# Optimization experiments

Hardware: AMD Instinct MI355X
Metric: run time of the kernel (lower is better)

The kernel has to match this reference:

```python
import jax, jax.numpy as jnp
import numpy as np

B, N, R, OUT = 8192, 4096, 16, 4096
STD = 0.01


def setup_inputs() -> dict:
    key = jax.random.key(0)
    ks = jax.random.split(key, 6)
    x = jax.random.normal(ks[0], (B, N), dtype=jnp.float32)
    G = STD * jax.random.normal(ks[1], (R, N), dtype=jnp.float32)
    H = STD * jax.random.normal(ks[2], (R, N), dtype=jnp.float32)
    b1 = STD * jax.random.normal(ks[3], (N,), dtype=jnp.float32)
    W2 = STD * jax.random.normal(ks[4], (N, OUT), dtype=jnp.float32)
    b2 = STD * jax.random.normal(ks[5], (OUT,), dtype=jnp.float32)
    return {"x": x, "G": G, "H": H, "b1": b1, "W2": W2, "b2": b2}


def reference(x, G, H, b1, W2, b2):
    # low-rank structured layer: xW = (x @ H^T) @ G  -- rank-r factorization of W
    xH = jnp.einsum('bn,rn->br', x, H)   # [B, r]
    xW = jnp.einsum('br,rn->bn', xH, G)  # [B, N]
    h = jax.nn.relu(xW + b1)             # num_layers == 1 branch
    y = jnp.matmul(h, W2) + b2           # [B, OUT]
    return y
```

## Files before the change

### kernel.cpp

```cpp
#include <hip/hip_runtime.h>
#include <hip/hip_bf16.h>
#include <cstdint>
#include <cstddef>

typedef __bf16 bf16;
typedef __bf16 bf16x4 __attribute__((ext_vector_type(4)));
typedef __bf16 bf16x8 __attribute__((ext_vector_type(8)));
typedef float  f32x4  __attribute__((ext_vector_type(4)));

#define MB   8192
#define NN   4096
#define RR   16
#define KOUT 4096

__device__ __forceinline__ void gload_lds16(const bf16* g, bf16* l) {
  __builtin_amdgcn_global_load_lds(
      (const __attribute__((address_space(1))) void*)g,
      (__attribute__((address_space(3))) void*)l, 16, 0, 0);
}

__global__ __launch_bounds__(256) void k1_lowrank(
    const float* __restrict__ x, const float* __restrict__ G,
    const float* __restrict__ H, const float* __restrict__ b1,
    bf16* __restrict__ hout)
{
  __shared__ float sS[16][16];
  const int t    = threadIdx.x;
  const int lane = t & 63;
  const int wave = t >> 6;
  const int r0   = blockIdx.x * 16;
  const int i0   = wave * 4;

  float acc[4][RR];
#pragma unroll
  for (int j = 0; j < 4; ++j)
#pragma unroll
    for (int r = 0; r < RR; ++r) acc[j][r] = 0.f;

  for (int kt = 0; kt < NN; kt += 256) {
    const int k = kt + lane * 4;
    f32x4 xv[4];
#pragma unroll
    for (int j = 0; j < 4; ++j)
      xv[j] = *(const f32x4*)(x + (size_t)(r0 + i0 + j) * NN + k);
#pragma unroll
    for (int r = 0; r < RR; ++r) {
      const f32x4 hv = *(const f32x4*)(H + (size_t)r * NN + k);
#pragma unroll
      for (int j = 0; j < 4; ++j) {
        acc[j][r] = fmaf(xv[j].x, hv.x, acc[j][r]);
        acc[j][r] = fmaf(xv[j].y, hv.y, acc[j][r]);
        acc[j][r] = fmaf(xv[j].z, hv.z, acc[j][r]);
        acc[j][r] = fmaf(xv[j].w, hv.w, acc[j][r]);
      }
    }
  }

#pragma unroll
  for (int j = 0; j < 4; ++j)
#pragma unroll
    for (int r = 0; r < RR; ++r) {
      float v = acc[j][r];
#pragma unroll
      for (int off = 32; off >= 1; off >>= 1) v += __shfl_xor(v, off, 64);
      acc[j][r] = v;
    }
  if (lane == 0) {
#pragma unroll
    for (int j = 0; j < 4; ++j)
#pragma unroll
      for (int r = 0; r < RR; ++r) sS[i0 + j][r] = acc[j][r];
  }
  __syncthreads();

#pragma unroll
  for (int chunk = 0; chunk < 4; ++chunk) {
    const int c = chunk * 1024 + t * 4;
    const f32x4 b1v = *(const f32x4*)(b1 + c);
#pragma unroll
    for (int ib = 0; ib < 16; ib += 4) {
      f32x4 a0 = {0.f,0.f,0.f,0.f}, a1 = a0, a2 = a0, a3 = a0;
#pragma unroll
      for (int rb = 0; rb < 16; rb += 4) {
        const f32x4 sv0 = *(const f32x4*)&sS[ib + 0][rb];
        const f32x4 sv1 = *(const f32x4*)&sS[ib + 1][rb];
        const f32x4 sv2 = *(const f32x4*)&sS[ib + 2][rb];
        const f32x4 sv3 = *(const f32x4*)&sS[ib + 3][rb];
#pragma unroll
        for (int rr = 0; rr < 4; ++rr) {
          const f32x4 g4 = *(const f32x4*)(G + (size_t)(rb + rr) * NN + c);
          a0 += sv0[rr] * g4;
          a1 += sv1[rr] * g4;
          a2 += sv2[rr] * g4;
          a3 += sv3[rr] * g4;
        }
      }
#define STORE_ROW(jj, av) {                                        \
      const f32x4 hv = (av) + b1v;                                 \
      bf16x4 o;                                                    \
      o[0] = (bf16)fmaxf(hv[0], 0.f); o[1] = (bf16)fmaxf(hv[1], 0.f); \
      o[2] = (bf16)fmaxf(hv[2], 0.f); o[3] = (bf16)fmaxf(hv[3], 0.f); \
      *(bf16x4*)(hout + (size_t)(r0 + ib + (jj)) * NN + c) = o; }
      STORE_ROW(0, a0) STORE_ROW(1, a1) STORE_ROW(2, a2) STORE_ROW(3, a3)
#undef STORE_ROW
    }
  }
}

__global__ __launch_bounds__(256) void k2_w2t(
    const float* __restrict__ W2, bf16* __restrict__ W2t)
{
  __shared__ float tile[64][65];
  const int t    = threadIdx.x;
  const int kb   = (blockIdx.x >> 6) * 64;
  const int ob   = (blockIdx.x & 63) * 64;
  const int row  = t >> 4;
  const int col4 = (t & 15) * 4;
#pragma unroll
  for (int p = 0; p < 4; ++p) {
    const f32x4 v = *(const f32x4*)(W2 + (size_t)(kb + p*16 + row) * KOUT + ob + col4);
    tile[p*16 + row][col4 + 0] = v[0];
    tile[p*16 + row][col4 + 1] = v[1];
    tile[p*16 + row][col4 + 2] = v[2];
    tile[p*16 + row][col4 + 3] = v[3];
  }
  __syncthreads();
  const int jj0 = t >> 4;
  const int ii4 = (t & 15) * 4;
#pragma unroll
  for (int p = 0; p < 4; ++p) {
    const int jj = p*16 + jj0;
    bf16x4 o;
    o[0] = (bf16)tile[ii4 + 0][jj];
    o[1] = (bf16)tile[ii4 + 1][jj];
    o[2] = (bf16)tile[ii4 + 2][jj];
    o[3] = (bf16)tile[ii4 + 3][jj];
    *(bf16x4*)(W2t + (size_t)(ob + jj) * NN + kb + ii4) = o;
  }
}

#define NT 64

__global__ __launch_bounds__(512, 1) void k3_gemm256(
    const bf16* __restrict__ A, const bf16* __restrict__ Bt,
    const float* __restrict__ b2, float* __restrict__ C)
{
  extern __shared__ __align__(16) char smem[];
  bf16* lds = (bf16*)smem;
  const char* ldsc = (const char*)smem;

  const int bid = blockIdx.x;
  const int swz = (bid & 7) * 64 + (bid >> 3);
  const int tm = swz >> 4, tn = swz & 15;
  const int brow = tm * 256, bcol = tn * 256;

  const int t    = threadIdx.x;
  const int lane = t & 63;
  const int wave = t >> 6;
  const int wr   = wave >> 2;
  const int wc   = wave & 3;
  const int fr   = lane & 15;
  const int fk   = lane >> 4;

  int srow[2], scol[2];
#pragma unroll
  for (int i = 0; i < 2; ++i) {
    const int d   = i * 8192 + t * 16;
    const int row = d >> 7;
    const int l   = d ^ ((row & 7) << 4);
    srow[i] = row;
    scol[i] = (l & 127) >> 1;
  }
  const bf16* gA0 = A  + (size_t)brow * NN;
  const bf16* gA1 = A  + (size_t)(brow + 128) * NN;
  const bf16* gB0 = Bt + (size_t)bcol * NN;
  const bf16* gB1 = Bt + (size_t)(bcol + 128) * NN;

  auto stage = [&](const bf16* g, int regionElem, int kt) {
#pragma unroll
    for (int i = 0; i < 2; ++i)
      gload_lds16(g + (size_t)srow[i] * NN + kt + scol[i],
                  lds + regionElem + i * 4096 + t * 8);
  };

  auto offA = [&](int mi, int kk) -> int {
    const int row = mi * 32 + wr * 16 + fr;
    const int b = row * 128 + kk * 64 + fk * 16;
    return b ^ ((row & 7) << 4);
  };
  auto offB = [&](int nj, int kk) -> int {
    const int row = nj * 64 + wc * 16 + fr;
    const int b = row * 128 + kk * 64 + fk * 16;
    return b ^ ((row & 7) << 4);
  };

  f32x4 acc[8][4];
#pragma unroll
  for (int m = 0; m < 8; ++m)
#pragma unroll
    for (int n = 0; n < 4; ++n) acc[m][n] = (f32x4){0.f,0.f,0.f,0.f};

  bf16x8 a[8], b0[4], b1[4];

  stage(gA0, 0,           0); stage(gB0, 32768,       0);
  stage(gB1, 32768+8192,  0); stage(gA1, 8192,        0);
  stage(gA0, 16384,       64); stage(gB0, 32768+16384, 64);
  stage(gB1, 32768+16384+8192, 64);
  asm volatile("s_waitcnt vmcnt(6)" ::: "memory");
  __builtin_amdgcn_s_barrier();
  asm volatile("" ::: "memory");
#pragma unroll
  for (int mi = 0; mi < 4; ++mi)
#pragma unroll
    for (int kk = 0; kk < 2; ++kk)
      a[mi*2+kk] = *(const bf16x8*)(ldsc + offA(mi, kk));
#pragma unroll
  for (int nj = 0; nj < 2; ++nj)
#pragma unroll
    for (int kk = 0; kk < 2; ++kk)
      b0[nj*2+kk] = *(const bf16x8*)(ldsc + 65536 + offB(nj, kk));

#pragma unroll 1
  for (int u0 = 0; u0 < NT; u0 += 2) {
#pragma unroll
    for (int hi = 0; hi < 2; ++hi) {
      const int u   = u0 + hi;
      const int buf = hi;
      const int obuf = buf ^ 1;
      const char* pa  = ldsc + buf  * 32768;
      const char* pb  = ldsc + 65536 + buf  * 32768;
      const char* pan = ldsc + obuf * 32768;
      const char* pbn = ldsc + 65536 + obuf * 32768;

      if (u < NT-1) stage(gA1, obuf*16384 + 8192, (u+1)*64);
      __builtin_amdgcn_s_barrier();
      __builtin_amdgcn_s_setprio(1);
#pragma unroll
      for (int mi = 0; mi < 4; ++mi)
#pragma unroll
        for (int nj = 0; nj < 2; ++nj)
#pragma unroll
          for (int kk = 0; kk < 2; ++kk)
            acc[mi][nj] = __builtin_amdgcn_mfma_f32_16x16x32_bf16(
                a[mi*2+kk], b0[nj*2+kk], acc[mi][nj], 0, 0, 0);
#pragma unroll
      for (int nj = 0; nj < 2; ++nj)
#pragma unroll
        for (int kk = 0; kk < 2; ++kk)
          b1[nj*2+kk] = *(const bf16x8*)(pb + 16384 + offB(nj, kk));
      __builtin_amdgcn_s_setprio(0);
      __builtin_amdgcn_s_barrier();

      if (u < NT-2) stage(gA0, buf*16384, (u+2)*64);
      __builtin_amdgcn_s_barrier();
      __builtin_amdgcn_s_setprio(1);
#pragma unroll
      for (int mi = 0; mi < 4; ++mi)
#pragma unroll
        for (int nj = 0; nj < 2; ++nj)
#pragma unroll
          for (int kk = 0; kk < 2; ++kk)
            acc[mi][2+nj] = __builtin_amdgcn_mfma_f32_16x16x32_bf16(
                a[mi*2+kk], b1[nj*2+kk], acc[mi][2+nj], 0, 0, 0);
#pragma unroll
      for (int mi = 0; mi < 4; ++mi)
#pragma unroll
        for (int kk = 0; kk < 2; ++kk)
          a[mi*2+kk] = *(const bf16x8*)(pa + 16384 + offA(mi, kk));
      __builtin_amdgcn_s_setprio(0);
      __builtin_amdgcn_s_barrier();

      if (u < NT-2) stage(gB0, 32768 + buf*16384, (u+2)*64);
      __builtin_amdgcn_s_barrier();
      __builtin_amdgcn_s_setprio(1);
#pragma unroll
      for (int mi = 0; mi < 4; ++mi)
#pragma unroll
        for (int nj = 0; nj < 2; ++nj)
#pragma unroll
          for (int kk = 0; kk < 2; ++kk)
            acc[4+mi][2+nj] = __builtin_amdgcn_mfma_f32_16x16x32_bf16(
                a[mi*2+kk], b1[nj*2+kk], acc[4+mi][2+nj], 0, 0, 0);
      __builtin_amdgcn_s_setprio(0);
      __builtin_amdgcn_s_barrier();

      if (u < NT-2) stage(gB1, 32768 + buf*16384 + 8192, (u+2)*64);
      if (u < NT-2)       { asm volatile("s_waitcnt vmcnt(6)" ::: "memory"); }
      else if (u == NT-2) { asm volatile("s_waitcnt vmcnt(0)" ::: "memory"); }
      __builtin_amdgcn_s_barrier();
      asm volatile("" ::: "memory");
      __builtin_amdgcn_s_setprio(1);
#pragma unroll
      for (int mi = 0; mi < 4; ++mi)
#pragma unroll
        for (int nj = 0; nj < 2; ++nj)
#pragma unroll
          for (int kk = 0; kk < 2; ++kk)
            acc[4+mi][nj] = __builtin_amdgcn_mfma_f32_16x16x32_bf16(
                a[mi*2+kk], b0[nj*2+kk], acc[4+mi][nj], 0, 0, 0);
      if (u < NT-1) {
#pragma unroll
        for (int mi = 0; mi < 4; ++mi)
#pragma unroll
          for (int kk = 0; kk < 2; ++kk)
            a[mi*2+kk] = *(const bf16x8*)(pan + offA(mi, kk));
#pragma unroll
        for (int nj = 0; nj < 2; ++nj)
#pragma unroll
          for (int kk = 0; kk < 2; ++kk)
            b0[nj*2+kk] = *(const bf16x8*)(pbn + offB(nj, kk));
      }
      __builtin_amdgcn_s_setprio(0);
      __builtin_amdgcn_s_barrier();
    }
  }

#pragma unroll
  for (int n = 0; n < 4; ++n) {
    const int col = bcol + n * 64 + wc * 16 + fr;
    const float bias = b2[col];
#pragma unroll
    for (int m = 0; m < 8; ++m) {
      const int row0 = brow + m * 32 + wr * 16 + fk * 4;
      float* cp = C + (size_t)row0 * KOUT + col;
#pragma unroll
      for (int q = 0; q < 4; ++q)
        cp[(size_t)q * KOUT] = acc[m][n][q] + bias;
    }
  }
}

extern "C" void kernel_launch(void* const* d_in, const int* in_sizes, int n_in,
                              void* d_out, int out_size, void* d_ws, size_t ws_size,
                              hipStream_t stream) {
  const float* x  = (const float*)d_in[0];
  const float* G  = (const float*)d_in[1];
  const float* H  = (const float*)d_in[2];
  const float* b1 = (const float*)d_in[3];
  const float* W2 = (const float*)d_in[4];
  const float* b2 = (const float*)d_in[5];
  float* y = (float*)d_out;

  bf16* hbuf = (bf16*)d_ws;
  bf16* w2t  = hbuf + (size_t)MB * NN;

  hipFuncSetAttribute((const void*)k3_gemm256,
                      hipFuncAttributeMaxDynamicSharedMemorySize, 131072);

  hipLaunchKernelGGL(k1_lowrank, dim3(MB / 16), dim3(256), 0, stream,
                     x, G, H, b1, hbuf);
  hipLaunchKernelGGL(k2_w2t, dim3(64 * 64), dim3(256), 0, stream, W2, w2t);
  hipLaunchKernelGGL(k3_gemm256, dim3((MB/256) * (KOUT/256)), dim3(512), 131072,
                     stream, hbuf, w2t, b2, y);
}
```

Baseline: 329.8 us.

## Split low-rank stage into MFMA xH kernel and expand kernel; trim GEMM barriers

```diff
diff --git a/kernel.cpp b/kernel.cpp
--- a/kernel.cpp
+++ b/kernel.cpp
@@ -7,103 +7,96 @@
 typedef __bf16 bf16x4 __attribute__((ext_vector_type(4)));
 typedef __bf16 bf16x8 __attribute__((ext_vector_type(8)));
 typedef float  f32x4  __attribute__((ext_vector_type(4)));
+typedef float  f32x8  __attribute__((ext_vector_type(8)));
 
 #define MB   8192
 #define NN   4096
 #define RR   16
 #define KOUT 4096
 
+#define FENCE() asm volatile("" ::: "memory")
+#define BARRIER() do { FENCE(); __builtin_amdgcn_s_barrier(); FENCE(); } while (0)
+
 __device__ __forceinline__ void gload_lds16(const bf16* g, bf16* l) {
   __builtin_amdgcn_global_load_lds(
       (const __attribute__((address_space(1))) void*)g,
       (__attribute__((address_space(3))) void*)l, 16, 0, 0);
 }
 
-__global__ __launch_bounds__(256) void k1_lowrank(
-    const float* __restrict__ x, const float* __restrict__ G,
-    const float* __restrict__ H, const float* __restrict__ b1,
-    bf16* __restrict__ hout)
+__global__ __launch_bounds__(256) void k1a_xh(
+    const float* __restrict__ x, const float* __restrict__ H,
+    float* __restrict__ xH)
 {
-  __shared__ float sS[16][16];
-  const int t    = threadIdx.x;
-  const int lane = t & 63;
-  const int wave = t >> 6;
-  const int r0   = blockIdx.x * 16;
-  const int i0   = wave * 4;
-
-  float acc[4][RR];
-#pragma unroll
-  for (int j = 0; j < 4; ++j)
-#pragma unroll
-    for (int r = 0; r < RR; ++r) acc[j][r] = 0.f;
-
-  for (int kt = 0; kt < NN; kt += 256) {
-    const int k = kt + lane * 4;
-    f32x4 xv[4];
-#pragma unroll
-    for (int j = 0; j < 4; ++j)
-      xv[j] = *(const f32x4*)(x + (size_t)(r0 + i0 + j) * NN + k);
-#pragma unroll
-    for (int r = 0; r < RR; ++r) {
-      const f32x4 hv = *(const f32x4*)(H + (size_t)r * NN + k);
-#pragma unroll
-      for (int j = 0; j < 4; ++j) {
-        acc[j][r] = fmaf(xv[j].x, hv.x, acc[j][r]);
-        acc[j][r] = fmaf(xv[j].y, hv.y, acc[j][r]);
-        acc[j][r] = fmaf(xv[j].z, hv.z, acc[j][r]);
-        acc[j][r] = fmaf(xv[j].w, hv.w, acc[j][r]);
-      }
+  __shared__ float red[4][64][4];
+  const int t = threadIdx.x, lane = t & 63, w = t >> 6;
+  const int r0 = blockIdx.x * 16;
+  const int fr = lane & 15, fk = lane >> 4;
+
+  const float* xp = x + (size_t)(r0 + fr) * NN + w * 1024 + fk * 8;
+  const float* hp = H + (size_t)fr * NN + w * 1024 + fk * 8;
+
+  f32x4 acc = {0.f, 0.f, 0.f, 0.f};
+#pragma unroll 4
+  for (int c = 0; c < 32; ++c) {
+    const f32x4 xa = *(const f32x4*)(xp + c * 32);
+    const f32x4 xb = *(const f32x4*)(xp + c * 32 + 4);
+    const f32x4 ha = *(const f32x4*)(hp + c * 32);
+    const f32x4 hb = *(const f32x4*)(hp + c * 32 + 4);
+    bf16x8 af, bfv;
+#pragma unroll
+    for (int j = 0; j < 4; ++j) {
+      af[j] = (bf16)xa[j]; af[4 + j] = (bf16)xb[j];
+      bfv[j] = (bf16)ha[j]; bfv[4 + j] = (bf16)hb[j];
     }
-  }
-
-#pragma unroll
-  for (int j = 0; j < 4; ++j)
-#pragma unroll
-    for (int r = 0; r < RR; ++r) {
-      float v = acc[j][r];
-#pragma unroll
-      for (int off = 32; off >= 1; off >>= 1) v += __shfl_xor(v, off, 64);
-      acc[j][r] = v;
+    acc = __builtin_amdgcn_mfma_f32_16x16x32_bf16(af, bfv, acc, 0, 0, 0);
+  }
+  *(f32x4*)&red[w][lane][0] = acc;
+  __syncthreads();
+  if (t < 64) {
+    f32x4 s = *(const f32x4*)&red[0][t][0];
+    s += *(const f32x4*)&red[1][t][0];
+    s += *(const f32x4*)&red[2][t][0];
+    s += *(const f32x4*)&red[3][t][0];
+#pragma unroll
+    for (int q = 0; q < 4; ++q)
+      xH[(size_t)(r0 + (t >> 4) * 4 + q) * RR + (t & 15)] = s[q];
+  }
+}
+
+__global__ __launch_bounds__(256) void k1b_h(
+    const float* __restrict__ xH, const float* __restrict__ G,
+    const float* __restrict__ b1, bf16* __restrict__ hout)
+{
+  const int t = threadIdx.x;
+  const int r0 = blockIdx.x * 4;
+
+  float xh[4][16];
+#pragma unroll
+  for (int row = 0; row < 4; ++row)
+#pragma unroll
+    for (int j = 0; j < 16; j += 4)
+      *(f32x4*)&xh[row][j] = *(const f32x4*)(xH + (size_t)(r0 + row) * RR + j);
+
+#pragma unroll
+  for (int half = 0; half < 2; ++half) {
+    const int col = half * 2048 + t * 8;
+    const f32x8 bv = *(const f32x8*)(b1 + col);
+    f32x8 a0 = bv, a1 = bv, a2 = bv, a3 = bv;
+#pragma unroll
+    for (int r = 0; r < 16; ++r) {
+      const f32x8 g8 = *(const f32x8*)(G + (size_t)r * NN + col);
+      a0 += xh[0][r] * g8;
+      a1 += xh[1][r] * g8;
+      a2 += xh[2][r] * g8;
+      a3 += xh[3][r] * g8;
     }
-  if (lane == 0) {
-#pragma unroll
-    for (int j = 0; j < 4; ++j)
-#pragma unroll
-      for (int r = 0; r < RR; ++r) sS[i0 + j][r] = acc[j][r];
-  }
-  __syncthreads();
-
-#pragma unroll
-  for (int chunk = 0; chunk < 4; ++chunk) {
-    const int c = chunk * 1024 + t * 4;
-    const f32x4 b1v = *(const f32x4*)(b1 + c);
-#pragma unroll
-    for (int ib = 0; ib < 16; ib += 4) {
-      f32x4 a0 = {0.f,0.f,0.f,0.f}, a1 = a0, a2 = a0, a3 = a0;
-#pragma unroll
-      for (int rb = 0; rb < 16; rb += 4) {
-        const f32x4 sv0 = *(const f32x4*)&sS[ib + 0][rb];
-        const f32x4 sv1 = *(const f32x4*)&sS[ib + 1][rb];
-        const f32x4 sv2 = *(const f32x4*)&sS[ib + 2][rb];
-        const f32x4 sv3 = *(const f32x4*)&sS[ib + 3][rb];
-#pragma unroll
-        for (int rr = 0; rr < 4; ++rr) {
-          const f32x4 g4 = *(const f32x4*)(G + (size_t)(rb + rr) * NN + c);
-          a0 += sv0[rr] * g4;
-          a1 += sv1[rr] * g4;
-          a2 += sv2[rr] * g4;
-          a3 += sv3[rr] * g4;
-        }
-      }
-#define STORE_ROW(jj, av) {                                        \
-      const f32x4 hv = (av) + b1v;                                 \
-      bf16x4 o;                                                    \
-      o[0] = (bf16)fmaxf(hv[0], 0.f); o[1] = (bf16)fmaxf(hv[1], 0.f); \
-      o[2] = (bf16)fmaxf(hv[2], 0.f); o[3] = (bf16)fmaxf(hv[3], 0.f); \
-      *(bf16x4*)(hout + (size_t)(r0 + ib + (jj)) * NN + c) = o; }
-      STORE_ROW(0, a0) STORE_ROW(1, a1) STORE_ROW(2, a2) STORE_ROW(3, a3)
+#define STORE_ROW(rr, av) {                                          \
+      bf16x8 o;                                                      \
+      _Pragma("unroll")                                              \
+      for (int j = 0; j < 8; ++j) o[j] = (bf16)fmaxf((av)[j], 0.f);  \
+      *(bf16x8*)(hout + (size_t)(r0 + (rr)) * NN + col) = o; }
+    STORE_ROW(0, a0) STORE_ROW(1, a1) STORE_ROW(2, a2) STORE_ROW(3, a3)
 #undef STORE_ROW
-    }
   }
 }
 
@@ -207,8 +200,7 @@
   stage(gA0, 16384,       64); stage(gB0, 32768+16384, 64);
   stage(gB1, 32768+16384+8192, 64);
   asm volatile("s_waitcnt vmcnt(6)" ::: "memory");
-  __builtin_amdgcn_s_barrier();
-  asm volatile("" ::: "memory");
+  BARRIER();
 #pragma unroll
   for (int mi = 0; mi < 4; ++mi)
 #pragma unroll
@@ -233,7 +225,6 @@
       const char* pbn = ldsc + 65536 + obuf * 32768;
 
       if (u < NT-1) stage(gA1, obuf*16384 + 8192, (u+1)*64);
-      __builtin_amdgcn_s_barrier();
       __builtin_amdgcn_s_setprio(1);
 #pragma unroll
       for (int mi = 0; mi < 4; ++mi)
@@ -249,10 +240,9 @@
         for (int kk = 0; kk < 2; ++kk)
           b1[nj*2+kk] = *(const bf16x8*)(pb + 16384 + offB(nj, kk));
       __builtin_amdgcn_s_setprio(0);
-      __builtin_amdgcn_s_barrier();
-
+
+      BARRIER();
       if (u < NT-2) stage(gA0, buf*16384, (u+2)*64);
-      __builtin_amdgcn_s_barrier();
       __builtin_amdgcn_s_setprio(1);
 #pragma unroll
       for (int mi = 0; mi < 4; ++mi)
@@ -268,10 +258,8 @@
         for (int kk = 0; kk < 2; ++kk)
           a[mi*2+kk] = *(const bf16x8*)(pa + 16384 + offA(mi, kk));
       __builtin_amdgcn_s_setprio(0);
-      __builtin_amdgcn_s_barrier();
 
       if (u < NT-2) stage(gB0, 32768 + buf*16384, (u+2)*64);
-      __builtin_amdgcn_s_barrier();
       __builtin_amdgcn_s_setprio(1);
 #pragma unroll
       for (int mi = 0; mi < 4; ++mi)
@@ -282,13 +270,11 @@
             acc[4+mi][2+nj] = __builtin_amdgcn_mfma_f32_16x16x32_bf16(
                 a[mi*2+kk], b1[nj*2+kk], acc[4+mi][2+nj], 0, 0, 0);
       __builtin_amdgcn_s_setprio(0);
-      __builtin_amdgcn_s_barrier();
 
       if (u < NT-2) stage(gB1, 32768 + buf*16384 + 8192, (u+2)*64);
       if (u < NT-2)       { asm volatile("s_waitcnt vmcnt(6)" ::: "memory"); }
       else if (u == NT-2) { asm volatile("s_waitcnt vmcnt(0)" ::: "memory"); }
-      __builtin_amdgcn_s_barrier();
-      asm volatile("" ::: "memory");
+      BARRIER();
       __builtin_amdgcn_s_setprio(1);
 #pragma unroll
       for (int mi = 0; mi < 4; ++mi)
@@ -311,7 +297,7 @@
             b0[nj*2+kk] = *(const bf16x8*)(pbn + offB(nj, kk));
       }
       __builtin_amdgcn_s_setprio(0);
-      __builtin_amdgcn_s_barrier();
+      BARRIER();
     }
   }
 
@@ -341,14 +327,15 @@
   const float* b2 = (const float*)d_in[5];
   float* y = (float*)d_out;
 
-  bf16* hbuf = (bf16*)d_ws;
-  bf16* w2t  = hbuf + (size_t)MB * NN;
+  bf16*  hbuf = (bf16*)d_ws;
+  bf16*  w2t  = hbuf + (size_t)MB * NN;
+  float* xhb  = (float*)(w2t + (size_t)NN * KOUT);
 
   hipFuncSetAttribute((const void*)k3_gemm256,
                       hipFuncAttributeMaxDynamicSharedMemorySize, 131072);
 
-  hipLaunchKernelGGL(k1_lowrank, dim3(MB / 16), dim3(256), 0, stream,
-                     x, G, H, b1, hbuf);
+  hipLaunchKernelGGL(k1a_xh, dim3(MB / 16), dim3(256), 0, stream, x, H, xhb);
+  hipLaunchKernelGGL(k1b_h,  dim3(MB / 4),  dim3(256), 0, stream, xhb, G, b1, hbuf);
   hipLaunchKernelGGL(k2_w2t, dim3(64 * 64), dim3(256), 0, stream, W2, w2t);
   hipLaunchKernelGGL(k3_gemm256, dim3((MB/256) * (KOUT/256)), dim3(512), 131072,
                      stream, hbuf, w2t, b2, y);
```

New measurement: 300.3 us. 8.9% less time.
